# Performance work log

Hardware: AMD Instinct MI355X
Metric: run time of the kernel (lower is better)

Reference implementation:

```python
import jax, jax.numpy as jnp
import numpy as np

OUT_H, OUT_W = 7, 7          # pooled output size
MAX_GRID = 4                 # static bound on adaptive sampling grid (ROI sizes <= 28 px)


def _axis_interp(pos, size, grid_mask):
    """torchvision bilinear rules along one axis.
    pos: sample coords, grid_mask: which adaptive-grid slots are active.
    Returns low/high indices and masked interpolation weights."""
    valid = (pos >= -1.0) & (pos <= size)          # outside -> contributes 0
    p = jnp.maximum(pos, 0.0)
    low = jnp.minimum(jnp.floor(p).astype(jnp.int32), size - 1)
    high = jnp.minimum(low + 1, size - 1)
    p = jnp.where(low >= size - 1, jnp.float32(size - 1), p)  # clamp at top edge
    frac = p - low.astype(p.dtype)
    m = (valid & grid_mask).astype(p.dtype)
    return low, high, (1.0 - frac) * m, frac * m


def _roi_align(features, rois):
    B, C, H, W = features.shape
    bidx = rois[:, 0].astype(jnp.int32)
    x1, y1, x2, y2 = rois[:, 1], rois[:, 2], rois[:, 3], rois[:, 4]
    # spatial_scale = 1.0, aligned=False -> min ROI size of 1
    roi_w = jnp.maximum(x2 - x1, 1.0)
    roi_h = jnp.maximum(y2 - y1, 1.0)
    bin_h = roi_h / OUT_H
    bin_w = roi_w / OUT_W
    # sampling_ratio = -1 -> adaptive grid = ceil(roi_size / pooled_size)
    gh = jnp.clip(jnp.ceil(roi_h / OUT_H).astype(jnp.int32), 1, MAX_GRID)
    gw = jnp.clip(jnp.ceil(roi_w / OUT_W).astype(jnp.int32), 1, MAX_GRID)
    g = jnp.arange(MAX_GRID)
    py = jnp.arange(OUT_H)
    px = jnp.arange(OUT_W)
    # sample coords: [N, OUT, MAX_GRID]
    ys = (y1[:, None, None] + py[None, :, None] * bin_h[:, None, None]
          + (g[None, None, :] + 0.5) * bin_h[:, None, None] / gh[:, None, None].astype(jnp.float32))
    xs = (x1[:, None, None] + px[None, :, None] * bin_w[:, None, None]
          + (g[None, None, :] + 0.5) * bin_w[:, None, None] / gw[:, None, None].astype(jnp.float32))
    gm_y = g[None, None, :] < gh[:, None, None]
    gm_x = g[None, None, :] < gw[:, None, None]
    y_lo, y_hi, wy0, wy1 = _axis_interp(ys, H, gm_y)
    x_lo, x_hi, wx0, wx1 = _axis_interp(xs, W, gm_x)

    f = features.reshape(B, C, H * W)
    bb = bidx[:, None, None, None, None]
    acc = jnp.zeros((rois.shape[0], OUT_H, OUT_W, C), dtype=features.dtype)
    # 4 bilinear corners; gather [N,OH,Gy,OW,Gx,C] one corner at a time
    for yi, wy in ((y_lo, wy0), (y_hi, wy1)):
        for xi, wx in ((x_lo, wx0), (x_hi, wx1)):
            idx = yi[:, :, :, None, None] * W + xi[:, None, None, :, :]  # [N,OH,Gy,OW,Gx]
            vals = f[bb, :, idx]                                         # [N,OH,Gy,OW,Gx,C]
            w = wy[:, :, :, None, None] * wx[:, None, None, :, :]
            acc = acc + jnp.einsum('nygxhc,nygxh->nyxc', vals, w)
    count = jnp.maximum(gh * gw, 1).astype(features.dtype)
    out = acc / count[:, None, None, None]
    return jnp.transpose(out, (0, 3, 1, 2))  # [N, C, OUT_H, OUT_W]


def setup_inputs() -> dict:
    key = jax.random.key(0)
    kf, kb, kx, ky, kw, kh = jax.random.split(key, 6)
    B, C, H, W, N = 4, 256, 200, 272, 512
    features = jax.random.normal(kf, (B, C, H, W), dtype=jnp.float32)
    b = jax.random.randint(kb, (N,), 0, B).astype(jnp.float32)
    # box sizes in [7, 28] px so adaptive grid ceil(size/7) <= MAX_GRID=4
    bw = jax.random.uniform(kw, (N,), minval=7.0, maxval=28.0)
    bh = jax.random.uniform(kh, (N,), minval=7.0, maxval=28.0)
    x1 = jax.random.uniform(kx, (N,), minval=0.0, maxval=W - 29.0)
    y1 = jax.random.uniform(ky, (N,), minval=0.0, maxval=H - 29.0)
    rois = jnp.stack([b, x1, y1, x1 + bw, y1 + bh], axis=1)
    return {"features": features, "rois": rois}


def reference(features, rois):
    return _roi_align(features, rois)
```

## Files before the change

### kernel.cpp

```cpp
#include <hip/hip_runtime.h>

#define MAXG 4
#define CPB 8
#define ROWS_MAX 30
#define LDS_STRIDE 37
#define CH_STRIDE (ROWS_MAX * LDS_STRIDE)

__global__ __launch_bounds__(512, 8) void roi_align_kernel(
    const float* __restrict__ feat,
    const float* __restrict__ rois,
    float* __restrict__ out,
    int C, int H, int W)
{
    const int n    = blockIdx.x;
    const int cblk = blockIdx.y;
    const int t    = threadIdx.x;

    __shared__ float s_feat[CPB * CH_STRIDE];
    __shared__ int4  s_ypack[28];
    __shared__ int4  s_xpack[28];

    const float* roi = rois + (size_t)n * 5;
    const int   b  = (int)roi[0];
    const float x1 = roi[1], y1 = roi[2], x2 = roi[3], y2 = roi[4];
    const float roi_w = fmaxf(x2 - x1, 1.0f);
    const float roi_h = fmaxf(y2 - y1, 1.0f);
    const float bin_h = roi_h / 7.0f;
    const float bin_w = roi_w / 7.0f;
    int gh = (int)ceilf(roi_h / 7.0f); gh = min(max(gh, 1), MAXG);
    int gw = (int)ceilf(roi_w / 7.0f); gw = min(max(gw, 1), MAXG);
    const float inv_count = 1.0f / (float)(gh * gw);

    auto lo_of = [](float pos, int size) {
        float p = fmaxf(pos, 0.0f);
        return min((int)floorf(p), size - 1);
    };
    const int y0 = lo_of(y1 + 0.5f * bin_h / (float)gh, H);
    const int yE = min(lo_of(y1 + 6.0f * bin_h + ((float)(gh - 1) + 0.5f) * bin_h / (float)gh, H) + 1, H - 1);
    const int x0 = lo_of(x1 + 0.5f * bin_w / (float)gw, W);
    const int xE = min(lo_of(x1 + 6.0f * bin_w + ((float)(gw - 1) + 0.5f) * bin_w / (float)gw, W) + 1, W - 1);
    const int rh    = min(yE - y0 + 1, ROWS_MAX);
    const int x0a   = x0 & ~3;
    const int spanA = min(xE - x0a + 1, 33);
    const int CM    = W - 4 - x0a;

    if (t < 28) {
        const int py = t >> 2, g = t & 3;
        float pos  = y1 + (float)py * bin_h + ((float)g + 0.5f) * bin_h / (float)gh;
        bool valid = (pos >= -1.0f) && (pos <= (float)H);
        float p = fmaxf(pos, 0.0f);
        int lo  = min((int)floorf(p), H - 1);
        int hi  = min(lo + 1, H - 1);
        if (lo >= H - 1) p = (float)(H - 1);
        float frac = p - (float)lo;
        float m = valid ? 1.0f : 0.0f;
        s_ypack[t] = make_int4((lo - y0) * LDS_STRIDE, (hi - y0) * LDS_STRIDE,
                               __float_as_int((1.0f - frac) * m),
                               __float_as_int(frac * m));
    } else if (t < 56) {
        const int u = t - 28;
        const int px = u >> 2, g = u & 3;
        float pos  = x1 + (float)px * bin_w + ((float)g + 0.5f) * bin_w / (float)gw;
        bool valid = (pos >= -1.0f) && (pos <= (float)W);
        float p = fmaxf(pos, 0.0f);
        int lo  = min((int)floorf(p), W - 1);
        int hi  = min(lo + 1, W - 1);
        if (lo >= W - 1) p = (float)(W - 1);
        float frac = p - (float)lo;
        float m = valid ? 1.0f : 0.0f;
        s_xpack[u] = make_int4(lo - x0a, hi - x0a,
                               __float_as_int((1.0f - frac) * m),
                               __float_as_int(frac * m));
    }

    const size_t HW = (size_t)H * W;
    const float* fbase = feat + ((size_t)b * C + cblk * CPB) * HW + (size_t)y0 * W + x0a;
    #pragma unroll
    for (int k = 0; k < 4; ++k) {
        const int s  = t + k * 512;
        const int ch = s >> 8;
        const int r  = (s >> 3) & 31;
        const int q  = s & 7;
        if (r < rh) {
            float* sp = s_feat + ch * CH_STRIDE + r * LDS_STRIDE;
            const float* gp = fbase + (size_t)ch * HW + (size_t)r * W;
            const int q4 = q << 2;
            if (q4 < spanA) {
                const int col = min(q4, CM);
                const float4 v = *(const float4*)(gp + col);
                sp[col + 0] = v.x; sp[col + 1] = v.y; sp[col + 2] = v.z; sp[col + 3] = v.w;
            }
            if (q == 7 && spanA == 33) {
                const int col = min(32, CM);
                const float4 v = *(const float4*)(gp + col);
                sp[col + 0] = v.x; sp[col + 1] = v.y; sp[col + 2] = v.z; sp[col + 3] = v.w;
            }
        }
    }
    __syncthreads();

    if (t < CPB * 49) {
        const int cl  = t / 49;
        const int pix = t - cl * 49;
        const int py  = pix / 7;
        const int px  = pix - py * 7;
        const float* sp = s_feat + cl * CH_STRIDE;

        int4 xp[4];
        #pragma unroll
        for (int g = 0; g < 4; ++g) xp[g] = s_xpack[(px << 2) + g];

        float acc = 0.0f;
        #pragma unroll
        for (int gy = 0; gy < MAXG; ++gy) {
            if (gy < gh) {
                const int4 yp = s_ypack[(py << 2) + gy];
                const float wy0 = __int_as_float(yp.z);
                const float wy1 = __int_as_float(yp.w);
                #pragma unroll
                for (int gx = 0; gx < MAXG; ++gx) {
                    if (gx < gw) {
                        const float wx0 = __int_as_float(xp[gx].z);
                        const float wx1 = __int_as_float(xp[gx].w);
                        const float v00 = sp[yp.x + xp[gx].x];
                        const float v01 = sp[yp.x + xp[gx].y];
                        const float v10 = sp[yp.y + xp[gx].x];
                        const float v11 = sp[yp.y + xp[gx].y];
                        acc += wy0 * (wx0 * v00 + wx1 * v01)
                             + wy1 * (wx0 * v10 + wx1 * v11);
                    }
                }
            }
        }
        out[((size_t)n * C + cblk * CPB) * 49 + t] = acc * inv_count;
    }
}

extern "C" void kernel_launch(void* const* d_in, const int* in_sizes, int n_in,
                              void* d_out, int out_size, void* d_ws, size_t ws_size,
                              hipStream_t stream) {
    const float* feat = (const float*)d_in[0];
    const float* rois = (const float*)d_in[1];
    float* out = (float*)d_out;

    const int C = 256, H = 200, W = 272;
    const int N = in_sizes[1] / 5;

    dim3 grid(N, C / CPB);
    roi_align_kernel<<<grid, 512, 0, stream>>>(feat, rois, out, C, H, W);
}
```

Before: 334.0 us.

## Process two channel chunks per block with register prefetch of the second chunk

Each block now handles 16 channels in two chunks of 8. The second chunk's global loads are issued into registers before the first chunk is computed, then written to LDS after a barrier. This halves the grid and amortizes the per-block ROI setup, and aims to hide global load latency behind compute. The cost is more registers (32 float4 prefetch values), extra barriers, and fewer blocks available for occupancy-based latency hiding.

```diff
diff --git a/kernel.cpp b/kernel.cpp
--- a/kernel.cpp
+++ b/kernel.cpp
@@ -2,6 +2,7 @@
 
 #define MAXG 4
 #define CPB 8
+#define NCHUNK 2
 #define ROWS_MAX 30
 #define LDS_STRIDE 37
 #define CH_STRIDE (ROWS_MAX * LDS_STRIDE)
@@ -73,67 +74,109 @@
                                __float_as_int(frac * m));
     }
 
+    const int  ch0    = t >> 8;
+    const int  r      = (t >> 3) & 31;
+    const int  q      = t & 7;
+    const int  q4     = q << 2;
+    const bool rowok  = r < rh;
+    const bool qok    = rowok && (q4 < spanA);
+    const bool tailok = rowok && (q == 7) && (spanA == 33);
+    const int  col    = min(q4, CM);
+    const int  colT   = min(32, CM);
+
     const size_t HW = (size_t)H * W;
-    const float* fbase = feat + ((size_t)b * C + cblk * CPB) * HW + (size_t)y0 * W + x0a;
-    #pragma unroll
-    for (int k = 0; k < 4; ++k) {
-        const int s  = t + k * 512;
-        const int ch = s >> 8;
-        const int r  = (s >> 3) & 31;
-        const int q  = s & 7;
-        if (r < rh) {
-            float* sp = s_feat + ch * CH_STRIDE + r * LDS_STRIDE;
-            const float* gp = fbase + (size_t)ch * HW + (size_t)r * W;
-            const int q4 = q << 2;
-            if (q4 < spanA) {
-                const int col = min(q4, CM);
+    const int c0A = cblk * (CPB * NCHUNK);
+    const int c0B = c0A + CPB;
+    const float* fbase = feat + ((size_t)b * C) * HW + (size_t)y0 * W + x0a;
+
+    {
+        const float* gp = fbase + (size_t)(c0A + ch0) * HW + (size_t)r * W;
+        float* sp = s_feat + ch0 * CH_STRIDE + r * LDS_STRIDE;
+        #pragma unroll
+        for (int k = 0; k < 4; ++k) {
+            if (qok) {
                 const float4 v = *(const float4*)(gp + col);
                 sp[col + 0] = v.x; sp[col + 1] = v.y; sp[col + 2] = v.z; sp[col + 3] = v.w;
             }
-            if (q == 7 && spanA == 33) {
-                const int col = min(32, CM);
-                const float4 v = *(const float4*)(gp + col);
-                sp[col + 0] = v.x; sp[col + 1] = v.y; sp[col + 2] = v.z; sp[col + 3] = v.w;
+            if (tailok) {
+                const float4 v = *(const float4*)(gp + colT);
+                sp[colT + 0] = v.x; sp[colT + 1] = v.y; sp[colT + 2] = v.z; sp[colT + 3] = v.w;
             }
+            gp += 2 * HW; sp += 2 * CH_STRIDE;
         }
     }
     __syncthreads();
 
-    if (t < CPB * 49) {
-        const int cl  = t / 49;
-        const int pix = t - cl * 49;
-        const int py  = pix / 7;
-        const int px  = pix - py * 7;
-        const float* sp = s_feat + cl * CH_STRIDE;
+    float4 pv[4], pvT[4];
+    {
+        const float* gp = fbase + (size_t)(c0B + ch0) * HW + (size_t)r * W;
+        #pragma unroll
+        for (int k = 0; k < 4; ++k) {
+            if (qok)    pv[k]  = *(const float4*)(gp + col);
+            if (tailok) pvT[k] = *(const float4*)(gp + colT);
+            gp += 2 * HW;
+        }
+    }
 
-        int4 xp[4];
-        #pragma unroll
-        for (int g = 0; g < 4; ++g) xp[g] = s_xpack[(px << 2) + g];
+    auto compute_chunk = [&](int c0) {
+        if (t < CPB * 49) {
+            const int cl  = t / 49;
+            const int pix = t - cl * 49;
+            const int py  = pix / 7;
+            const int px  = pix - py * 7;
+            const float* sp = s_feat + cl * CH_STRIDE;
 
-        float acc = 0.0f;
-        #pragma unroll
-        for (int gy = 0; gy < MAXG; ++gy) {
-            if (gy < gh) {
-                const int4 yp = s_ypack[(py << 2) + gy];
-                const float wy0 = __int_as_float(yp.z);
-                const float wy1 = __int_as_float(yp.w);
-                #pragma unroll
-                for (int gx = 0; gx < MAXG; ++gx) {
-                    if (gx < gw) {
-                        const float wx0 = __int_as_float(xp[gx].z);
-                        const float wx1 = __int_as_float(xp[gx].w);
-                        const float v00 = sp[yp.x + xp[gx].x];
-                        const float v01 = sp[yp.x + xp[gx].y];
-                        const float v10 = sp[yp.y + xp[gx].x];
-                        const float v11 = sp[yp.y + xp[gx].y];
-                        acc += wy0 * (wx0 * v00 + wx1 * v01)
-                             + wy1 * (wx0 * v10 + wx1 * v11);
+            int4 xp[4];
+            #pragma unroll
+            for (int g = 0; g < 4; ++g) xp[g] = s_xpack[(px << 2) + g];
+
+            float acc = 0.0f;
+            #pragma unroll
+            for (int gy = 0; gy < MAXG; ++gy) {
+                if (gy < gh) {
+                    const int4 yp = s_ypack[(py << 2) + gy];
+                    const float wy0 = __int_as_float(yp.z);
+                    const float wy1 = __int_as_float(yp.w);
+                    #pragma unroll
+                    for (int gx = 0; gx < MAXG; ++gx) {
+                        if (gx < gw) {
+                            const float wx0 = __int_as_float(xp[gx].z);
+                            const float wx1 = __int_as_float(xp[gx].w);
+                            const float v00 = sp[yp.x + xp[gx].x];
+                            const float v01 = sp[yp.x + xp[gx].y];
+                            const float v10 = sp[yp.y + xp[gx].x];
+                            const float v11 = sp[yp.y + xp[gx].y];
+                            acc += wy0 * (wx0 * v00 + wx1 * v01)
+                                 + wy1 * (wx0 * v10 + wx1 * v11);
+                        }
                     }
                 }
             }
+            out[((size_t)n * C + c0) * 49 + t] = acc * inv_count;
         }
-        out[((size_t)n * C + cblk * CPB) * 49 + t] = acc * inv_count;
+    };
+
+    compute_chunk(c0A);
+    __syncthreads();
+
+    {
+        float* sp = s_feat + ch0 * CH_STRIDE + r * LDS_STRIDE;
+        #pragma unroll
+        for (int k = 0; k < 4; ++k) {
+            if (qok) {
+                sp[col + 0] = pv[k].x; sp[col + 1] = pv[k].y;
+                sp[col + 2] = pv[k].z; sp[col + 3] = pv[k].w;
+            }
+            if (tailok) {
+                sp[colT + 0] = pvT[k].x; sp[colT + 1] = pvT[k].y;
+                sp[colT + 2] = pvT[k].z; sp[colT + 3] = pvT[k].w;
+            }
+            sp += 2 * CH_STRIDE;
+        }
     }
+    __syncthreads();
+
+    compute_chunk(c0B);
 }
 
 extern "C" void kernel_launch(void* const* d_in, const int* in_sizes, int n_in,
@@ -146,6 +189,6 @@
     const int C = 256, H = 200, W = 272;
     const int N = in_sizes[1] / 5;
 
-    dim3 grid(N, C / CPB);
+    dim3 grid(N, C / (CPB * NCHUNK));
     roi_align_kernel<<<grid, 512, 0, stream>>>(feat, rois, out, C, H, W);
 }
```

Result: no change. 335.5 us (+0.5%).

## Interleave channel pairs in LDS as float2 and halve block size

Applied to the files above, without the earlier changes.

Changes the shared-memory layout so that pairs of channels are stored interleaved as float2 with a padded stride. Each compute thread now produces two channels with one 64-bit LDS read per corner instead of two 32-bit reads. The block shrinks from 512 to 256 threads, with fewer but wider loads per thread. This cuts LDS instruction count and per-block index math, at the cost of fewer active threads in compute (196) and a more complex load mapping.

```diff
diff --git a/kernel.cpp b/kernel.cpp
--- a/kernel.cpp
+++ b/kernel.cpp
@@ -2,11 +2,12 @@
 
 #define MAXG 4
 #define CPB 8
-#define ROWS_MAX 30
-#define LDS_STRIDE 37
-#define CH_STRIDE (ROWS_MAX * LDS_STRIDE)
+#define UCOLS 33
+#define PSTRIDE 5
+#define YMUL (UCOLS * PSTRIDE)
+#define S2LEN ((29 * UCOLS + 32) * PSTRIDE + 8)
 
-__global__ __launch_bounds__(512, 8) void roi_align_kernel(
+__global__ __launch_bounds__(256, 4) void roi_align_kernel(
     const float* __restrict__ feat,
     const float* __restrict__ rois,
     float* __restrict__ out,
@@ -16,9 +17,9 @@
     const int cblk = blockIdx.y;
     const int t    = threadIdx.x;
 
-    __shared__ float s_feat[CPB * CH_STRIDE];
-    __shared__ int4  s_ypack[28];
-    __shared__ int4  s_xpack[28];
+    __shared__ float2 s_feat2[S2LEN];
+    __shared__ int4   s_ypack[28];
+    __shared__ int4   s_xpack[28];
 
     const float* roi = rois + (size_t)n * 5;
     const int   b  = (int)roi[0];
@@ -39,7 +40,7 @@
     const int yE = min(lo_of(y1 + 6.0f * bin_h + ((float)(gh - 1) + 0.5f) * bin_h / (float)gh, H) + 1, H - 1);
     const int x0 = lo_of(x1 + 0.5f * bin_w / (float)gw, W);
     const int xE = min(lo_of(x1 + 6.0f * bin_w + ((float)(gw - 1) + 0.5f) * bin_w / (float)gw, W) + 1, W - 1);
-    const int rh    = min(yE - y0 + 1, ROWS_MAX);
+    const int rh    = min(yE - y0 + 1, 30);
     const int x0a   = x0 & ~3;
     const int spanA = min(xE - x0a + 1, 33);
     const int CM    = W - 4 - x0a;
@@ -54,7 +55,7 @@
         if (lo >= H - 1) p = (float)(H - 1);
         float frac = p - (float)lo;
         float m = valid ? 1.0f : 0.0f;
-        s_ypack[t] = make_int4((lo - y0) * LDS_STRIDE, (hi - y0) * LDS_STRIDE,
+        s_ypack[t] = make_int4((lo - y0) * YMUL, (hi - y0) * YMUL,
                                __float_as_int((1.0f - frac) * m),
                                __float_as_int(frac * m));
     } else if (t < 56) {
@@ -68,49 +69,60 @@
         if (lo >= W - 1) p = (float)(W - 1);
         float frac = p - (float)lo;
         float m = valid ? 1.0f : 0.0f;
-        s_xpack[u] = make_int4(lo - x0a, hi - x0a,
+        s_xpack[u] = make_int4((lo - x0a) * PSTRIDE, (hi - x0a) * PSTRIDE,
                                __float_as_int((1.0f - frac) * m),
                                __float_as_int(frac * m));
     }
 
-    const size_t HW = (size_t)H * W;
-    const float* fbase = feat + ((size_t)b * C + cblk * CPB) * HW + (size_t)y0 * W + x0a;
-    #pragma unroll
-    for (int k = 0; k < 4; ++k) {
-        const int s  = t + k * 512;
-        const int ch = s >> 8;
-        const int r  = (s >> 3) & 31;
-        const int q  = s & 7;
-        if (r < rh) {
-            float* sp = s_feat + ch * CH_STRIDE + r * LDS_STRIDE;
-            const float* gp = fbase + (size_t)ch * HW + (size_t)r * W;
-            const int q4 = q << 2;
-            if (q4 < spanA) {
-                const int col = min(q4, CM);
-                const float4 v = *(const float4*)(gp + col);
-                sp[col + 0] = v.x; sp[col + 1] = v.y; sp[col + 2] = v.z; sp[col + 3] = v.w;
-            }
-            if (q == 7 && spanA == 33) {
-                const int col = min(32, CM);
-                const float4 v = *(const float4*)(gp + col);
-                sp[col + 0] = v.x; sp[col + 1] = v.y; sp[col + 2] = v.z; sp[col + 3] = v.w;
+    {
+        const int  p    = t & 3;
+        const int  q    = (t >> 2) & 7;
+        const int  r0   = t >> 5;
+        const int  q4   = q << 2;
+        const bool qon  = (q4 < spanA);
+        const int  colA = min(q4, CM);
+        const bool tail = (q == 7) && (spanA == 33);
+
+        const size_t HW = (size_t)H * W;
+        const int c0 = cblk * CPB;
+        const float* fbase = feat + ((size_t)b * C + c0) * HW + (size_t)y0 * W + x0a;
+        const float* ga = fbase + (size_t)(2 * p) * HW;
+        float2* sb = s_feat2 + p;
+
+        #pragma unroll
+        for (int k = 0; k < 4; ++k) {
+            const int r = r0 + (k << 3);
+            if (r < rh) {
+                const float* gp = ga + (size_t)r * W;
+                if (qon) {
+                    const float4 va = *(const float4*)(gp + colA);
+                    const float4 vb = *(const float4*)(gp + HW + colA);
+                    float2* sp = sb + (r * UCOLS + colA) * PSTRIDE;
+                    sp[0]           = make_float2(va.x, vb.x);
+                    sp[PSTRIDE]     = make_float2(va.y, vb.y);
+                    sp[2 * PSTRIDE] = make_float2(va.z, vb.z);
+                    sp[3 * PSTRIDE] = make_float2(va.w, vb.w);
+                }
+                if (tail) {
+                    sb[(r * UCOLS + 32) * PSTRIDE] = make_float2(gp[32], gp[HW + 32]);
+                }
             }
         }
     }
     __syncthreads();
 
-    if (t < CPB * 49) {
-        const int cl  = t / 49;
-        const int pix = t - cl * 49;
+    if (t < 196) {
+        const int p   = t & 3;
+        const int pix = t >> 2;
         const int py  = pix / 7;
         const int px  = pix - py * 7;
-        const float* sp = s_feat + cl * CH_STRIDE;
+        const float2* sp = s_feat2 + p;
 
         int4 xp[4];
         #pragma unroll
         for (int g = 0; g < 4; ++g) xp[g] = s_xpack[(px << 2) + g];
 
-        float acc = 0.0f;
+        float ax = 0.0f, ay = 0.0f;
         #pragma unroll
         for (int gy = 0; gy < MAXG; ++gy) {
             if (gy < gh) {
@@ -122,17 +134,21 @@
                     if (gx < gw) {
                         const float wx0 = __int_as_float(xp[gx].z);
                         const float wx1 = __int_as_float(xp[gx].w);
-                        const float v00 = sp[yp.x + xp[gx].x];
-                        const float v01 = sp[yp.x + xp[gx].y];
-                        const float v10 = sp[yp.y + xp[gx].x];
-                        const float v11 = sp[yp.y + xp[gx].y];
-                        acc += wy0 * (wx0 * v00 + wx1 * v01)
-                             + wy1 * (wx0 * v10 + wx1 * v11);
+                        const float2 v00 = sp[yp.x + xp[gx].x];
+                        const float2 v01 = sp[yp.x + xp[gx].y];
+                        const float2 v10 = sp[yp.y + xp[gx].x];
+                        const float2 v11 = sp[yp.y + xp[gx].y];
+                        ax += wy0 * (wx0 * v00.x + wx1 * v01.x)
+                            + wy1 * (wx0 * v10.x + wx1 * v11.x);
+                        ay += wy0 * (wx0 * v00.y + wx1 * v01.y)
+                            + wy1 * (wx0 * v10.y + wx1 * v11.y);
                     }
                 }
             }
         }
-        out[((size_t)n * C + cblk * CPB) * 49 + t] = acc * inv_count;
+        const size_t ob = ((size_t)n * C + cblk * CPB + 2 * p) * 49 + pix;
+        out[ob]      = ax * inv_count;
+        out[ob + 49] = ay * inv_count;
     }
 }
 
@@ -147,5 +163,5 @@
     const int N = in_sizes[1] / 5;
 
     dim3 grid(N, C / CPB);
-    roi_align_kernel<<<grid, 512, 0, stream>>>(feat, rois, out, C, H, W);
+    roi_align_kernel<<<grid, 256, 0, stream>>>(feat, rois, out, C, H, W);
 }
```

Result: faster. 324.0 us (-3.0%).
